# Kernel tuning notes

Measured on AMD Instinct MI355X. Metric: run time of the kernel, lower is better.

The kernel has to match this reference:

```python
import jax, jax.numpy as jnp
import numpy as np

N_NODES = 50000
N_EDGES = 800000
D = 128


def setup_inputs() -> dict:
    key = jax.random.key(0)
    k1, k2, k3, k4, k5 = jax.random.split(key, 5)
    node_attr = jax.random.normal(k1, (N_NODES, D), dtype=jnp.float32)
    edge_index = jax.random.randint(k2, (2, N_EDGES), 0, N_NODES, dtype=jnp.int64)
    edge_attr = jax.random.normal(k3, (N_EDGES, D), dtype=jnp.float32)
    # 2-layer MLP: (3D -> D) -> ReLU -> (D -> D), scaled init
    w1 = jax.random.normal(k4, (3 * D, D), dtype=jnp.float32) * (1.0 / np.sqrt(3 * D))
    b1 = jnp.zeros((D,), dtype=jnp.float32)
    w2 = jax.random.normal(k5, (D, D), dtype=jnp.float32) * (1.0 / np.sqrt(D))
    b2 = jnp.zeros((D,), dtype=jnp.float32)
    return {"node_attr": node_attr, "edge_index": edge_index, "edge_attr": edge_attr,
            "w1": w1, "b1": b1, "w2": w2, "b2": b2}


def reference(node_attr, edge_index, edge_attr, w1, b1, w2, b2):
    senders_idx = edge_index[0]
    receivers_idx = edge_index[1]
    senders_attr = node_attr[senders_idx]      # [E, D] irregular gather
    receivers_attr = node_attr[receivers_idx]  # [E, D] irregular gather
    collected = jnp.concatenate([senders_attr, receivers_attr, edge_attr], axis=1)  # [E, 3D]
    h = jax.nn.relu(collected @ w1 + b1)       # [E, D]
    edge_attr_new = h @ w2 + b2                # [E, D]
    return edge_attr_new
```

## Files before the change

### kernel.cpp

```cpp
#include <hip/hip_runtime.h>


#define NE 800000
#define ND 50000
#define DD 128

typedef float f32x4v __attribute__((ext_vector_type(4)));
typedef float f32x4a __attribute__((ext_vector_type(4)));
typedef _Float16 f16x8 __attribute__((ext_vector_type(8)));
typedef _Float16 f16x4 __attribute__((ext_vector_type(4)));

__device__ __forceinline__ f16x4 cvt4(f32x4v v) {
    f16x4 r;
    r[0] = (_Float16)v[0]; r[1] = (_Float16)v[1];
    r[2] = (_Float16)v[2]; r[3] = (_Float16)v[3];
    return r;
}

__global__ void prep_w(const float* __restrict__ w1, const float* __restrict__ w2,
                       _Float16* __restrict__ w1t, _Float16* __restrict__ w2f) {
    int i = blockIdx.x * 256 + threadIdx.x;
    if (i < 384 * 128) {
        int col = i / 384;
        int k = i - col * 384;
        float v = w1[(size_t)k * 128 + col];
        int byteoff = col * 768 + ((k * 2) ^ ((col & 15) << 4));
        *(_Float16*)((char*)w1t + byteoff) = (_Float16)v;
    } else {
        int j = i - 384 * 128;
        int ks = j >> 10;
        int col = (j >> 3) & 127;
        int jj = j & 7;
        w2f[j] = (_Float16)w2[(size_t)(ks * 8 + jj) * 128 + col];
    }
}

__global__ void prep_node(const float* __restrict__ node_attr, _Float16* __restrict__ nf16) {
    int i = blockIdx.x * 256 + threadIdx.x;
    const float* src = node_attr + (size_t)i * 8;
    f32x4v a = *(const f32x4v*)src;
    f32x4v b = *(const f32x4v*)(src + 4);
    f16x8 r;
    r[0] = (_Float16)a[0]; r[1] = (_Float16)a[1];
    r[2] = (_Float16)a[2]; r[3] = (_Float16)a[3];
    r[4] = (_Float16)b[0]; r[5] = (_Float16)b[1];
    r[6] = (_Float16)b[2]; r[7] = (_Float16)b[3];
    *(f16x8*)(nf16 + (size_t)i * 8) = r;
}

#define MFMA_SEG(SEG)                                                                     \
    _Pragma("unroll")                                                                     \
    for (int kk = 0; kk < 4; kk++) {                                                      \
        f16x8 a = *(const f16x8*)(ab + r15 * 256 + ((kk * 64 + q16) ^ xa));               \
        _Pragma("unroll")                                                                 \
        for (int n = 0; n < 8; n++) {                                                     \
            const int col = n * 16 + r15;                                                 \
            f16x8 b = *(const f16x8*)(lds + col * 768 +                                   \
                       ((((SEG) * 4 + kk) * 64 + q16) ^ xa));                             \
            acc[n] = __builtin_amdgcn_mfma_f32_16x16x32_f16(a, b, acc[n], 0, 0, 0);       \
        }                                                                                 \
    }

#define WRITE_SEG16(V)                                                                    \
    _Pragma("unroll")                                                                     \
    for (int i = 0; i < 8; i++) {                                                         \
        const int row = 2 * i + sub;                                                      \
        *(f16x4*)(ab + row * 256 + ((c31 * 8) ^ ((row & 15) << 4))) = V[i];               \
    }

__global__ __attribute__((amdgpu_flat_work_group_size(768, 768),
                          amdgpu_waves_per_eu(3, 3)))
void edge_mlp(
    const float* __restrict__ node_attr,
    const int* __restrict__ eidx,
    const float* __restrict__ edge_attr,
    const _Float16* __restrict__ w1t,
    const float* __restrict__ b1,
    const _Float16* __restrict__ w2f,
    const float* __restrict__ b2,
    const _Float16* __restrict__ nf16,
    float* __restrict__ out) {
    extern __shared__ char lds[];

    const int tid = threadIdx.x;
    const int wid = tid >> 6;
    const int lane = tid & 63;
    const int r15 = lane & 15;
    const int q16 = (lane >> 4) * 16;
    const int sub = lane >> 5;
    const int c31 = lane & 31;

    {
        const char* src = (const char*)w1t;
        #pragma unroll
        for (int i = 0; i < 8; i++) {
            int off = (tid + i * 768) * 16;
            *(f16x8*)(lds + off) = *(const f16x8*)(src + off);
        }
    }

    float b1v[8], b2v[8];
    #pragma unroll
    for (int n = 0; n < 8; n++) { b1v[n] = b1[n * 16 + r15]; b2v[n] = b2[n * 16 + r15]; }

    __syncthreads();

    char* ab = lds + 96 * 1024 + wid * 4096;
    const int xa = r15 << 4;
    int ebase = blockIdx.x * 192 + wid * 16;
    if (ebase > NE - 16) ebase = NE - 16;

    const int sidx = eidx[ebase + r15];
    const int ridx = eidx[NE + ebase + r15];

    f16x4 sv[8];
    #pragma unroll
    for (int i = 0; i < 8; i++) {
        int r = __shfl(sidx, 2 * i + sub);
        sv[i] = *(const f16x4*)(nf16 + (size_t)r * DD + c31 * 4);
    }
    WRITE_SEG16(sv)

    f16x4 rv[8];
    #pragma unroll
    for (int i = 0; i < 8; i++) {
        int r = __shfl(ridx, 2 * i + sub);
        rv[i] = *(const f16x4*)(nf16 + (size_t)r * DD + c31 * 4);
    }

    f32x4a acc[8] = {};
    __builtin_amdgcn_wave_barrier();

    MFMA_SEG(0)

    WRITE_SEG16(rv)
    f32x4v ev[8];
    #pragma unroll
    for (int i = 0; i < 8; i++) {
        const int row = 2 * i + sub;
        ev[i] = __builtin_nontemporal_load(
            (const f32x4v*)(edge_attr + (size_t)(ebase + row) * DD + c31 * 4));
    }
    __builtin_amdgcn_wave_barrier();

    MFMA_SEG(1)

    #pragma unroll
    for (int i = 0; i < 8; i++) {
        const int row = 2 * i + sub;
        *(f16x4*)(ab + row * 256 + ((c31 * 8) ^ ((row & 15) << 4))) = cvt4(ev[i]);
    }
    f16x8 b2fa[2][8];
    #pragma unroll
    for (int kk = 0; kk < 2; kk++)
        #pragma unroll
        for (int n = 0; n < 8; n++) {
            const int ks = kk * 4 + (lane >> 4);
            b2fa[kk][n] = *(const f16x8*)(w2f + ((size_t)(ks * 128 + n * 16 + r15)) * 8);
        }
    __builtin_amdgcn_wave_barrier();

    MFMA_SEG(2)

    #pragma unroll
    for (int n = 0; n < 8; n++) {
        const int col = n * 16 + r15;
        #pragma unroll
        for (int reg = 0; reg < 4; reg++) {
            const int row = (lane >> 4) * 4 + reg;
            float v = fmaxf(acc[n][reg] + b1v[n], 0.0f);
            *(_Float16*)(ab + row * 256 + ((col * 2) ^ ((row & 15) << 4))) = (_Float16)v;
        }
    }
    __builtin_amdgcn_wave_barrier();

    f32x4a acc2[8] = {};
    #pragma unroll
    for (int kk = 0; kk < 2; kk++) {
        f16x8 a = *(const f16x8*)(ab + r15 * 256 + ((kk * 64 + q16) ^ xa));
        #pragma unroll
        for (int n = 0; n < 8; n++)
            acc2[n] = __builtin_amdgcn_mfma_f32_16x16x32_f16(a, b2fa[kk][n], acc2[n], 0, 0, 0);
    }
    f16x8 b2fb[2][8];
    #pragma unroll
    for (int kk = 0; kk < 2; kk++)
        #pragma unroll
        for (int n = 0; n < 8; n++) {
            const int ks = (kk + 2) * 4 + (lane >> 4);
            b2fb[kk][n] = *(const f16x8*)(w2f + ((size_t)(ks * 128 + n * 16 + r15)) * 8);
        }
    #pragma unroll
    for (int kk = 2; kk < 4; kk++) {
        f16x8 a = *(const f16x8*)(ab + r15 * 256 + ((kk * 64 + q16) ^ xa));
        #pragma unroll
        for (int n = 0; n < 8; n++)
            acc2[n] = __builtin_amdgcn_mfma_f32_16x16x32_f16(a, b2fb[kk - 2][n], acc2[n], 0, 0, 0);
    }

    #pragma unroll
    for (int n = 0; n < 8; n++) {
        #pragma unroll
        for (int reg = 0; reg < 4; reg++) {
            const int row = (lane >> 4) * 4 + reg;
            out[(size_t)(ebase + row) * DD + n * 16 + r15] = acc2[n][reg] + b2v[n];
        }
    }
}

extern "C" void kernel_launch(void* const* d_in, const int* in_sizes, int n_in,
                              void* d_out, int out_size, void* d_ws, size_t ws_size,
                              hipStream_t stream) {
    const float* node_attr = (const float*)d_in[0];
    const int* eidx = (const int*)d_in[1];
    const float* edge_attr = (const float*)d_in[2];
    const float* w1 = (const float*)d_in[3];
    const float* b1 = (const float*)d_in[4];
    const float* w2 = (const float*)d_in[5];
    const float* b2 = (const float*)d_in[6];
    float* out = (float*)d_out;

    _Float16* w1t = (_Float16*)d_ws;
    _Float16* w2f = w1t + 384 * 128;
    _Float16* nf16 = w2f + 128 * 128;

    hipFuncSetAttribute((const void*)edge_mlp,
                        hipFuncAttributeMaxDynamicSharedMemorySize, 160 * 1024);

    prep_w<<<256, 256, 0, stream>>>(w1, w2, w1t, w2f);
    prep_node<<<3125, 256, 0, stream>>>(node_attr, nf16);
    edge_mlp<<<4167, 768, 144 * 1024, stream>>>(node_attr, eidx, edge_attr,
                                                w1t, b1, w2f, b2, nf16, out);
}
```

Before: 273.2 us.

## Process four edge tiles per wave with direct-to-LDS gathers and double buffering

```diff
diff --git a/kernel.cpp b/kernel.cpp
--- a/kernel.cpp
+++ b/kernel.cpp
@@ -2,7 +2,6 @@
 
 
 #define NE 800000
-#define ND 50000
 #define DD 128
 
 typedef float f32x4v __attribute__((ext_vector_type(4)));
@@ -48,10 +47,10 @@
     *(f16x8*)(nf16 + (size_t)i * 8) = r;
 }
 
-#define MFMA_SEG(SEG)                                                                     \
+#define MFMA_SEG(BUF, SEG)                                                                \
     _Pragma("unroll")                                                                     \
     for (int kk = 0; kk < 4; kk++) {                                                      \
-        f16x8 a = *(const f16x8*)(ab + r15 * 256 + ((kk * 64 + q16) ^ xa));               \
+        f16x8 a = *(const f16x8*)((BUF) + r15 * 256 + ((kk * 64 + q16) ^ xa));            \
         _Pragma("unroll")                                                                 \
         for (int n = 0; n < 8; n++) {                                                     \
             const int col = n * 16 + r15;                                                 \
@@ -61,15 +60,8 @@
         }                                                                                 \
     }
 
-#define WRITE_SEG16(V)                                                                    \
-    _Pragma("unroll")                                                                     \
-    for (int i = 0; i < 8; i++) {                                                         \
-        const int row = 2 * i + sub;                                                      \
-        *(f16x4*)(ab + row * 256 + ((c31 * 8) ^ ((row & 15) << 4))) = V[i];               \
-    }
-
-__global__ __attribute__((amdgpu_flat_work_group_size(768, 768),
-                          amdgpu_waves_per_eu(3, 3)))
+__global__ __attribute__((amdgpu_flat_work_group_size(512, 512),
+                          amdgpu_waves_per_eu(2, 2)))
 void edge_mlp(
     const float* __restrict__ node_attr,
     const int* __restrict__ eidx,
@@ -89,12 +81,24 @@
     const int q16 = (lane >> 4) * 16;
     const int sub = lane >> 5;
     const int c31 = lane & 31;
+    const int xa = r15 << 4;
+
+    const int gb = blockIdx.x * 512 + wid * 64;
+    int eb[4]; int sid[4]; int rid[4];
+    #pragma unroll
+    for (int t = 0; t < 4; t++) {
+        int e = gb + t * 16;
+        if (e > NE - 16) e = NE - 16;
+        eb[t] = e;
+        sid[t] = eidx[e + r15];
+        rid[t] = eidx[NE + e + r15];
+    }
 
     {
         const char* src = (const char*)w1t;
         #pragma unroll
-        for (int i = 0; i < 8; i++) {
-            int off = (tid + i * 768) * 16;
+        for (int i = 0; i < 12; i++) {
+            int off = (tid + i * 512) * 16;
             *(f16x8*)(lds + off) = *(const f16x8*)(src + off);
         }
     }
@@ -105,107 +109,122 @@
 
     __syncthreads();
 
-    char* ab = lds + 96 * 1024 + wid * 4096;
-    const int xa = r15 << 4;
-    int ebase = blockIdx.x * 192 + wid * 16;
-    if (ebase > NE - 16) ebase = NE - 16;
-
-    const int sidx = eidx[ebase + r15];
-    const int ridx = eidx[NE + ebase + r15];
-
-    f16x4 sv[8];
-    #pragma unroll
-    for (int i = 0; i < 8; i++) {
-        int r = __shfl(sidx, 2 * i + sub);
-        sv[i] = *(const f16x4*)(nf16 + (size_t)r * DD + c31 * 4);
-    }
-    WRITE_SEG16(sv)
-
-    f16x4 rv[8];
-    #pragma unroll
-    for (int i = 0; i < 8; i++) {
-        int r = __shfl(ridx, 2 * i + sub);
-        rv[i] = *(const f16x4*)(nf16 + (size_t)r * DD + c31 * 4);
-    }
-
-    f32x4a acc[8] = {};
-    __builtin_amdgcn_wave_barrier();
-
-    MFMA_SEG(0)
-
-    WRITE_SEG16(rv)
-    f32x4v ev[8];
-    #pragma unroll
-    for (int i = 0; i < 8; i++) {
-        const int row = 2 * i + sub;
-        ev[i] = __builtin_nontemporal_load(
-            (const f32x4v*)(edge_attr + (size_t)(ebase + row) * DD + c31 * 4));
-    }
-    __builtin_amdgcn_wave_barrier();
-
-    MFMA_SEG(1)
-
-    #pragma unroll
-    for (int i = 0; i < 8; i++) {
-        const int row = 2 * i + sub;
-        *(f16x4*)(ab + row * 256 + ((c31 * 8) ^ ((row & 15) << 4))) = cvt4(ev[i]);
-    }
-    f16x8 b2fa[2][8];
-    #pragma unroll
-    for (int kk = 0; kk < 2; kk++)
-        #pragma unroll
-        for (int n = 0; n < 8; n++) {
-            const int ks = kk * 4 + (lane >> 4);
-            b2fa[kk][n] = *(const f16x8*)(w2f + ((size_t)(ks * 128 + n * 16 + r15)) * 8);
-        }
-    __builtin_amdgcn_wave_barrier();
-
-    MFMA_SEG(2)
-
-    #pragma unroll
-    for (int n = 0; n < 8; n++) {
-        const int col = n * 16 + r15;
-        #pragma unroll
-        for (int reg = 0; reg < 4; reg++) {
-            const int row = (lane >> 4) * 4 + reg;
-            float v = fmaxf(acc[n][reg] + b1v[n], 0.0f);
-            *(_Float16*)(ab + row * 256 + ((col * 2) ^ ((row & 15) << 4))) = (_Float16)v;
-        }
-    }
-    __builtin_amdgcn_wave_barrier();
-
-    f32x4a acc2[8] = {};
-    #pragma unroll
-    for (int kk = 0; kk < 2; kk++) {
-        f16x8 a = *(const f16x8*)(ab + r15 * 256 + ((kk * 64 + q16) ^ xa));
-        #pragma unroll
-        for (int n = 0; n < 8; n++)
-            acc2[n] = __builtin_amdgcn_mfma_f32_16x16x32_f16(a, b2fa[kk][n], acc2[n], 0, 0, 0);
-    }
-    f16x8 b2fb[2][8];
-    #pragma unroll
-    for (int kk = 0; kk < 2; kk++)
-        #pragma unroll
-        for (int n = 0; n < 8; n++) {
-            const int ks = (kk + 2) * 4 + (lane >> 4);
-            b2fb[kk][n] = *(const f16x8*)(w2f + ((size_t)(ks * 128 + n * 16 + r15)) * 8);
-        }
-    #pragma unroll
-    for (int kk = 2; kk < 4; kk++) {
-        f16x8 a = *(const f16x8*)(ab + r15 * 256 + ((kk * 64 + q16) ^ xa));
-        #pragma unroll
-        for (int n = 0; n < 8; n++)
-            acc2[n] = __builtin_amdgcn_mfma_f32_16x16x32_f16(a, b2fb[kk - 2][n], acc2[n], 0, 0, 0);
-    }
-
-    #pragma unroll
-    for (int n = 0; n < 8; n++) {
-        #pragma unroll
-        for (int reg = 0; reg < 4; reg++) {
-            const int row = (lane >> 4) * 4 + reg;
-            out[(size_t)(ebase + row) * DD + n * 16 + r15] = acc2[n][reg] + b2v[n];
-        }
-    }
+    char* ab0 = lds + 96 * 1024 + wid * 8192;
+    char* ab1 = ab0 + 4096;
+
+#define GATHER_SEG(IDX, BUF)                                                              \
+    {                                                                                     \
+        _Pragma("unroll")                                                                 \
+        for (int j = 0; j < 4; j++) {                                                     \
+            const int row = 4 * j + (lane >> 4);                                          \
+            const int rr = __shfl((IDX), row);                                            \
+            const int q = (lane & 15) * 16;                                               \
+            const char* srcp = (const char*)(nf16 + (size_t)rr * DD)                      \
+                               + (q ^ ((row & 15) << 4));                                 \
+            __builtin_amdgcn_global_load_lds(                                             \
+                (const __attribute__((address_space(1))) void*)srcp,                      \
+                (__attribute__((address_space(3))) void*)((BUF) + j * 1024),              \
+                16, 0, 0);                                                                \
+        }                                                                                 \
+    }
+
+    GATHER_SEG(sid[0], ab0)
+    asm volatile("s_waitcnt vmcnt(0)" ::: "memory");
+
+#define TILE_BODY(T, BS, BR, DO_NEXT, NBUF)                                               \
+    {                                                                                     \
+        const int ebase = eb[T];                                                          \
+        GATHER_SEG(rid[T], BR)                                          \
+        f32x4v ev[8];                                                                     \
+        _Pragma("unroll")                                                                 \
+        for (int i = 0; i < 8; i++) {                                             \
+            const int row = 2 * i + sub;                                                  \
+            ev[i] = __builtin_nontemporal_load(                                           \
+                (const f32x4v*)(edge_attr + (size_t)(ebase + row) * DD + c31 * 4));       \
+        }                                                                                 \
+           \
+        asm volatile("s_waitcnt vmcnt(44)" ::: "memory");                                 \
+        __builtin_amdgcn_sched_barrier(0);                                                \
+        f32x4a acc[8] = {};                                                               \
+        __builtin_amdgcn_wave_barrier();                                                  \
+        MFMA_SEG(BS, 0)                                                                   \
+                              \
+        _Pragma("unroll")                                                                 \
+        for (int i = 0; i < 8; i++) {                                                     \
+            const int row = 2 * i + sub;                                                  \
+            *(f16x4*)((BS) + row * 256 + ((c31 * 8) ^ ((row & 15) << 4))) = cvt4(ev[i]);  \
+        }                                                                                 \
+        asm volatile("s_waitcnt vmcnt(0)" ::: "memory");       \
+        __builtin_amdgcn_sched_barrier(0);                                                \
+        __builtin_amdgcn_wave_barrier();                                                  \
+        MFMA_SEG(BR, 1)                                                                   \
+        __builtin_amdgcn_wave_barrier();                                                  \
+        MFMA_SEG(BS, 2)                                                                   \
+                                                                \
+        _Pragma("unroll")                                                                 \
+        for (int n = 0; n < 8; n++) {                                                     \
+            const int col = n * 16 + r15;                                                 \
+            _Pragma("unroll")                                                             \
+            for (int reg = 0; reg < 4; reg++) {                                           \
+                const int row = (lane >> 4) * 4 + reg;                                    \
+                float v = fmaxf(acc[n][reg] + b1v[n], 0.0f);                              \
+                *(_Float16*)((BS) + row * 256 + ((col * 2) ^ ((row & 15) << 4))) =        \
+                    (_Float16)v;                                                          \
+            }                                                                             \
+        }                                                                                 \
+        __builtin_amdgcn_wave_barrier();                                                  \
+                                                                               \
+        f32x4a acc2[8] = {};                                                              \
+        f16x8 b2fa[2][8];                                                                 \
+        _Pragma("unroll")                                                                 \
+        for (int kk = 0; kk < 2; kk++)                                                    \
+            _Pragma("unroll")                                                             \
+            for (int n = 0; n < 8; n++) {                                                 \
+                const int ks = kk * 4 + (lane >> 4);                                      \
+                b2fa[kk][n] = *(const f16x8*)(w2f + ((size_t)(ks * 128 + n * 16 + r15)) * 8); \
+            }                                                                             \
+        _Pragma("unroll")                                                                 \
+        for (int kk = 0; kk < 2; kk++) {                                                  \
+            f16x8 a = *(const f16x8*)((BS) + r15 * 256 + ((kk * 64 + q16) ^ xa));         \
+            _Pragma("unroll")                                                             \
+            for (int n = 0; n < 8; n++)                                                   \
+                acc2[n] = __builtin_amdgcn_mfma_f32_16x16x32_f16(a, b2fa[kk][n], acc2[n], 0, 0, 0); \
+        }                                                                                 \
+        f16x8 b2fb[2][8];                                                                 \
+        _Pragma("unroll")                                                                 \
+        for (int kk = 0; kk < 2; kk++)                                                    \
+            _Pragma("unroll")                                                             \
+            for (int n = 0; n < 8; n++) {                                                 \
+                const int ks = (kk + 2) * 4 + (lane >> 4);                                \
+                b2fb[kk][n] = *(const f16x8*)(w2f + ((size_t)(ks * 128 + n * 16 + r15)) * 8); \
+            }                                                                             \
+        _Pragma("unroll")                                                                 \
+        for (int kk = 2; kk < 4; kk++) {                                                  \
+            f16x8 a = *(const f16x8*)((BS) + r15 * 256 + ((kk * 64 + q16) ^ xa));         \
+            _Pragma("unroll")                                                             \
+            for (int n = 0; n < 8; n++)                                                   \
+                acc2[n] = __builtin_amdgcn_mfma_f32_16x16x32_f16(a, b2fb[kk - 2][n], acc2[n], 0, 0, 0); \
+        }                                                                                 \
+                                        \
+        if (DO_NEXT) { GATHER_SEG(sid[(T) + 1], NBUF) }                                   \
+        asm volatile("" ::: "memory");                                                    \
+                                   \
+        _Pragma("unroll")                                                                 \
+        for (int n = 0; n < 8; n++) {                                                     \
+            _Pragma("unroll")                                                             \
+            for (int reg = 0; reg < 4; reg++) {                                           \
+                const int row = (lane >> 4) * 4 + reg;                                    \
+                __builtin_nontemporal_store(acc2[n][reg] + b2v[n],                        \
+                    out + (size_t)(ebase + row) * DD + n * 16 + r15);                     \
+            }                                                                             \
+        }                                                                                 \
+        asm volatile("" ::: "memory");                                                    \
+    }
+
+    TILE_BODY(0, ab0, ab1, 1, ab1)
+    TILE_BODY(1, ab1, ab0, 1, ab0)
+    TILE_BODY(2, ab0, ab1, 1, ab1)
+    TILE_BODY(3, ab1, ab0, 0, ab0)
 }
 
 extern "C" void kernel_launch(void* const* d_in, const int* in_sizes, int n_in,
@@ -229,6 +248,6 @@
 
     prep_w<<<256, 256, 0, stream>>>(w1, w2, w1t, w2f);
     prep_node<<<3125, 256, 0, stream>>>(node_attr, nf16);
-    edge_mlp<<<4167, 768, 144 * 1024, stream>>>(node_attr, eidx, edge_attr,
+    edge_mlp<<<1563, 512, 160 * 1024, stream>>>(node_attr, eidx, edge_attr,
                                                 w1t, b1, w2f, b2, nf16, out);
 }
```

Measured after the change: 433.1 us. 1.59x slower.
